# Kernel tuning notes

Measured on AMD Instinct MI355X. Metric: run time of the kernel, lower is better.

The kernel has to match this reference:

```python
import jax, jax.numpy as jnp
import numpy as np

N_NODES = 50000
N_EDGES = 800000
IN_CH = 128
OUT_CH = 64
HEADS = 2
NEG_SLOPE = 0.2


def _gat_conv(x, src, dst, W, a_src, a_dst, b, n):
    """PyG-style GATConv (eval mode: no dropout), self-loops already appended.
    x: [n, F_in]; W: [F_in, H*C]; a_src/a_dst: [H, C]; b: [H*C]."""
    H, C = a_src.shape
    h = (x @ W).reshape(n, H, C)                       # [n, H, C]
    alpha_src = jnp.sum(h * a_src, axis=-1)            # [n, H]
    alpha_dst = jnp.sum(h * a_dst, axis=-1)            # [n, H]
    e = alpha_src[src] + alpha_dst[dst]                # [E, H]
    e = jnp.where(e > 0, e, NEG_SLOPE * e)             # LeakyReLU(0.2)
    # neighbor-wise (destination-grouped) softmax, numerically stable
    m = jax.ops.segment_max(e, dst, num_segments=n)
    e = jnp.exp(e - m[dst])
    denom = jax.ops.segment_sum(e, dst, num_segments=n)
    alpha = e / (denom[dst] + 1e-16)                   # [E, H]
    out = jax.ops.segment_sum(alpha[:, :, None] * h[src], dst, num_segments=n)
    return out.reshape(n, H * C) + b


def setup_inputs() -> dict:
    key = jax.random.key(0)
    ks = jax.random.split(key, 12)
    s = 0.08  # glorot-ish scale
    x = jax.random.normal(ks[0], (N_NODES, IN_CH), dtype=jnp.float32)
    edge_index = jax.random.randint(ks[1], (2, N_EDGES), 0, N_NODES, dtype=jnp.int64)
    H, O = HEADS, OUT_CH
    return {
        "x": x,
        "edge_index": edge_index,
        "W1": jax.random.normal(ks[2], (IN_CH, H * 2 * O), dtype=jnp.float32) * s,
        "a_src1": jax.random.normal(ks[3], (H, 2 * O), dtype=jnp.float32) * s,
        "a_dst1": jax.random.normal(ks[4], (H, 2 * O), dtype=jnp.float32) * s,
        "b1": jnp.zeros((H * 2 * O,), dtype=jnp.float32),
        "W_mu": jax.random.normal(ks[5], (2 * O * H, H * O), dtype=jnp.float32) * s,
        "a_src_mu": jax.random.normal(ks[6], (H, O), dtype=jnp.float32) * s,
        "a_dst_mu": jax.random.normal(ks[7], (H, O), dtype=jnp.float32) * s,
        "b_mu": jnp.zeros((H * O,), dtype=jnp.float32),
        "W_ls": jax.random.normal(ks[8], (2 * O * H, H * O), dtype=jnp.float32) * s,
        "a_src_ls": jax.random.normal(ks[9], (H, O), dtype=jnp.float32) * s,
        "a_dst_ls": jax.random.normal(ks[10], (H, O), dtype=jnp.float32) * s,
        "b_ls": jnp.zeros((H * O,), dtype=jnp.float32),
    }


def reference(x, edge_index, W1, a_src1, a_dst1, b1,
              W_mu, a_src_mu, a_dst_mu, b_mu,
              W_ls, a_src_ls, a_dst_ls, b_ls):
    n = x.shape[0]
    loop = jnp.arange(n, dtype=edge_index.dtype)
    src = jnp.concatenate([edge_index[0], loop])  # PyG add_self_loops=True
    dst = jnp.concatenate([edge_index[1], loop])
    x1 = jax.nn.elu(_gat_conv(x, src, dst, W1, a_src1, a_dst1, b1, n))
    mu = _gat_conv(x1, src, dst, W_mu, a_src_mu, a_dst_mu, b_mu, n)
    logstd = _gat_conv(x1, src, dst, W_ls, a_src_ls, a_dst_ls, b_ls, n)
    return (mu, logstd)
```

## Files before the change

### kernel.cpp

```cpp
#include <hip/hip_runtime.h>


typedef unsigned short u16;
typedef unsigned int u32;
typedef _Float16 f16;
typedef f16 f16x8 __attribute__((ext_vector_type(8)));
typedef float f32x4v __attribute__((ext_vector_type(4)));

__device__ __forceinline__ u16 f2h(float f) {
    union { f16 h; u16 u; } t;
    t.h = (f16)f;
    return t.u;
}
__device__ __forceinline__ float4 loadh4(const u16* __restrict__ p, size_t i) {
    union { uint2 u; f16 h[4]; } t;
    t.u = *(const uint2*)(p + i);
    return make_float4((float)t.h[0], (float)t.h[1], (float)t.h[2], (float)t.h[3]);
}
__device__ __forceinline__ void store4(float* __restrict__ p, size_t i, float4 v) {
    *(float4*)(p + i) = v;
}
__device__ __forceinline__ void store4(u16* __restrict__ p, size_t i, float4 v) {
    union { uint2 u; f16 h[4]; } t;
    t.h[0] = (f16)v.x; t.h[1] = (f16)v.y; t.h[2] = (f16)v.z; t.h[3] = (f16)v.w;
    *(uint2*)(p + i) = t.u;
}

__global__ __launch_bounds__(256) void k_detect(const u32* __restrict__ ebuf,
                                                int* __restrict__ flag) {
    __shared__ int nz;
    if (threadIdx.x == 0) nz = 0;
    __syncthreads();
    if (ebuf[2 * threadIdx.x + 1] != 0u) atomicAdd(&nz, 1);
    __syncthreads();
    if (threadIdx.x == 0) *flag = (nz == 0) ? 1 : 0;
}

__global__ __launch_bounds__(256) void k_extract(const u32* __restrict__ ebuf, int E,
                                                 const int* __restrict__ flag,
                                                 int* __restrict__ se,
                                                 int* __restrict__ de,
                                                 int* __restrict__ deg) {
    int e = blockIdx.x * 256 + threadIdx.x;
    if (e >= E) return;
    int s, d;
    if (*flag) {
        s = (int)ebuf[2 * (size_t)e];
        d = (int)ebuf[2 * ((size_t)E + (size_t)e)];
    } else {
        s = (int)ebuf[e];
        d = (int)ebuf[(size_t)E + (size_t)e];
    }
    se[e] = s;
    de[e] = d;
    atomicAdd(&deg[d], 1);
}

__global__ __launch_bounds__(256) void k_scan_a(const int* __restrict__ deg, int n,
                                                int* __restrict__ bsum) {
    __shared__ int s[256];
    int i = blockIdx.x * 256 + threadIdx.x;
    s[threadIdx.x] = (i < n) ? deg[i] : 0;
    __syncthreads();
    for (int st = 128; st > 0; st >>= 1) {
        if (threadIdx.x < st) s[threadIdx.x] += s[threadIdx.x + st];
        __syncthreads();
    }
    if (threadIdx.x == 0) bsum[blockIdx.x] = s[0];
}

__global__ __launch_bounds__(256) void k_scan_b(int* __restrict__ bsum, int nb) {
    __shared__ int s[256];
    int t = threadIdx.x;
    int v = (t < nb) ? bsum[t] : 0;
    s[t] = v;
    __syncthreads();
    for (int off = 1; off < 256; off <<= 1) {
        int add = (t >= off) ? s[t - off] : 0;
        __syncthreads();
        s[t] += add;
        __syncthreads();
    }
    if (t < nb) bsum[t] = s[t] - v;
}

__global__ __launch_bounds__(256) void k_scan_c(const int* __restrict__ deg, int n,
                                                const int* __restrict__ bsum,
                                                int* __restrict__ rowptr,
                                                int* __restrict__ cursor, int E) {
    __shared__ int s[256];
    int t = threadIdx.x;
    int i = blockIdx.x * 256 + t;
    int v = (i < n) ? deg[i] : 0;
    s[t] = v;
    __syncthreads();
    for (int off = 1; off < 256; off <<= 1) {
        int add = (t >= off) ? s[t - off] : 0;
        __syncthreads();
        s[t] += add;
        __syncthreads();
    }
    if (i < n) {
        int ex = bsum[blockIdx.x] + s[t] - v;
        rowptr[i] = ex;
        cursor[i] = ex;
    }
    if (i == 0) rowptr[n] = E;
}

__global__ __launch_bounds__(256) void k_fill(const int* __restrict__ src,
                                              const int* __restrict__ dst, int E,
                                              int* __restrict__ cursor,
                                              int* __restrict__ csr_src,
                                              int* __restrict__ csr_dst) {
    int e = blockIdx.x * 256 + threadIdx.x;
    if (e < E) {
        int d = dst[e];
        int slot = atomicAdd(&cursor[d], 1);
        csr_src[slot] = src[e];
        csr_dst[slot] = d;
    }
}

__global__ __launch_bounds__(256) void k_cvt(const float* __restrict__ in,
                                             u16* __restrict__ out, int nElem) {
    int i = (blockIdx.x * 256 + threadIdx.x) * 4;
    if (i >= nElem) return;
    float4 v = *(const float4*)(in + i);
    store4(out, i, v);
}

__global__ __launch_bounds__(256) void k_tw(const float* __restrict__ Wl,
                                            const float* __restrict__ Wr, int split,
                                            int K, u16* __restrict__ Wt) {
    int idx = blockIdx.x * 256 + threadIdx.x;
    if (idx >= 256 * K) return;
    int c = idx / K, k = idx - c * K;
    float v;
    if (split == 256)
        v = Wl[(size_t)k * 256 + c];
    else
        v = (c < 128) ? Wl[(size_t)k * 128 + c] : Wr[(size_t)k * 128 + (c - 128)];
    Wt[idx] = f2h(v);
}

template <int NS>
__global__ __launch_bounds__(256) void k_w(const int* __restrict__ csr_src,
                                           const int* __restrict__ csr_dst,
                                           const float* __restrict__ as,
                                           const float* __restrict__ ad,
                                           float* __restrict__ wp, int E) {
    int i = blockIdx.x * 256 + threadIdx.x;
    if (i >= E) return;
    int s = csr_src[i], d = csr_dst[i];
    if (NS == 2) {
        float2 a = *(const float2*)(as + (size_t)s * 2);
        float2 b = *(const float2*)(ad + (size_t)d * 2);
        float e0 = a.x + b.x, e1 = a.y + b.y;
        e0 = fmaxf(e0, 0.2f * e0);
        e1 = fmaxf(e1, 0.2f * e1);
        wp[i] = __expf(e0);
        wp[(size_t)E + i] = __expf(e1);
    } else {
        float4 a = *(const float4*)(as + (size_t)s * 4);
        float4 b = *(const float4*)(ad + (size_t)d * 4);
        float e0 = a.x + b.x, e1 = a.y + b.y, e2 = a.z + b.z, e3 = a.w + b.w;
        e0 = fmaxf(e0, 0.2f * e0);
        e1 = fmaxf(e1, 0.2f * e1);
        e2 = fmaxf(e2, 0.2f * e2);
        e3 = fmaxf(e3, 0.2f * e3);
        wp[i] = __expf(e0);
        wp[(size_t)E + i] = __expf(e1);
        wp[2 * (size_t)E + i] = __expf(e2);
        wp[3 * (size_t)E + i] = __expf(e3);
    }
}

template <int K, int ALOGW>
__global__ __launch_bounds__(256) void k_gemm_mfma(
    const u16* __restrict__ Ah, const u16* __restrict__ Wt, u16* __restrict__ out,
    float* __restrict__ as_out, float* __restrict__ ad_out,
    const float* __restrict__ alo, const float* __restrict__ ahi,
    const float* __restrict__ dlo, const float* __restrict__ dhi, int M) {
    __shared__ u16 Bs[256 * 40];
    const int tid = threadIdx.x;
    const int wave = tid >> 6;
    const int lane = tid & 63;
    const int li = lane & 15;
    const int quad = lane >> 4;
    const int r0 = blockIdx.x * 64 + wave * 16;
    int arowi = r0 + li;
    if (arowi >= M) arowi = M - 1;
    const u16* arow = Ah + (size_t)arowi * K + quad * 8;

    f32x4v acc[16];
#pragma unroll
    for (int ct = 0; ct < 16; ct++) acc[ct] = (f32x4v)(0.f);

    for (int t = 0; t < K; t += 32) {
        __syncthreads();
        {
            const u16* src = Wt + (size_t)tid * K + t;
            u16* dst = Bs + tid * 40;
            uint4 v0 = ((const uint4*)src)[0];
            uint4 v1 = ((const uint4*)src)[1];
            uint4 v2 = ((const uint4*)src)[2];
            uint4 v3 = ((const uint4*)src)[3];
            ((uint4*)dst)[0] = v0;
            ((uint4*)(dst + 8))[0] = v1;
            ((uint4*)(dst + 16))[0] = v2;
            ((uint4*)(dst + 24))[0] = v3;
        }
        __syncthreads();
        f16x8 a = *(const f16x8*)(arow + t);
#pragma unroll
        for (int ct = 0; ct < 16; ct++) {
            f16x8 b = *(const f16x8*)(Bs + (ct * 16 + li) * 40 + quad * 8);
            acc[ct] = __builtin_amdgcn_mfma_f32_16x16x32_f16(a, b, acc[ct], 0, 0, 0);
        }
    }

#pragma unroll
    for (int reg = 0; reg < 4; reg++) {
        int grow = r0 + quad * 4 + reg;
        if (grow < M) {
            u16* orow = out + (size_t)grow * 256 + li;
#pragma unroll
            for (int ct = 0; ct < 16; ct++) orow[ct * 16] = f2h(acc[ct][reg]);
        }
    }

    const int NS = 64 >> ALOGW;
    const int SH = ALOGW - 2;
    float aw[16], dw[16];
#pragma unroll
    for (int ct = 0; ct < 16; ct++) {
        int col = ct * 16 + li;
        aw[ct] = (col < 128) ? alo[col] : ahi[col - 128];
        dw[ct] = (col < 128) ? dlo[col] : dhi[col - 128];
    }
#pragma unroll
    for (int reg = 0; reg < 4; reg++) {
        float s[4] = {0.f, 0.f, 0.f, 0.f};
        float d[4] = {0.f, 0.f, 0.f, 0.f};
#pragma unroll
        for (int ct = 0; ct < 16; ct++) {
            int sl = ct >> SH;
            s[sl] += acc[ct][reg] * aw[ct];
            d[sl] += acc[ct][reg] * dw[ct];
        }
#pragma unroll
        for (int sl = 0; sl < NS; sl++) {
#pragma unroll
            for (int m = 1; m <= 8; m <<= 1) {
                s[sl] += __shfl_xor(s[sl], m, 64);
                d[sl] += __shfl_xor(d[sl], m, 64);
            }
        }
        int grow = r0 + quad * 4 + reg;
        if (li == 0 && grow < M) {
#pragma unroll
            for (int sl = 0; sl < NS; sl++) {
                as_out[(size_t)grow * NS + sl] = s[sl];
                ad_out[(size_t)grow * NS + sl] = d[sl];
            }
        }
    }
}

template <int LOGW, int MODE, typename OT>
__global__ __launch_bounds__(256) void k_agg4(
    const u16* __restrict__ h, const int* __restrict__ rowptr,
    const int* __restrict__ csr_src, const float* __restrict__ wp,
    const float* __restrict__ as, const float* __restrict__ ad,
    const float* __restrict__ b_lo, const float* __restrict__ b_hi,
    OT* __restrict__ outp, int n, int nGrp, int E) {
    const int NS = 64 >> LOGW;
    const int bid = blockIdx.x;
    const int xcd = bid & 7;
    const int half = xcd >> 2;
    const int grp = (bid >> 3) * 4 + (xcd & 3);
    if (grp >= nGrp) return;
    const int lane = threadIdx.x & 63;
    const int sub = lane >> 5;
    const int sl = lane & 31;
    const int wid0 = grp * 8 + (threadIdx.x >> 6) * 2 + sub;
    const bool ok = wid0 < n;
    const int wid = ok ? wid0 : (n - 1);
    const int col = half * 128 + sl * 4;
    const int slot = col >> (LOGW + 2);
    const float* __restrict__ wpl = wp + (size_t)slot * E;

    float e = as[(size_t)wid * NS + slot] + ad[(size_t)wid * NS + slot];
    e = fmaxf(e, 0.2f * e);
    float w = __expf(e);
    float denom = w;
    float4 hv = loadh4(h, (size_t)wid * 256 + col);
    float acc0 = w * hv.x, acc1 = w * hv.y, acc2 = w * hv.z, acc3 = w * hv.w;

    int rb = 0, re = 0;
    if (ok) { rb = rowptr[wid0]; re = rowptr[wid0 + 1]; }
    int p = rb;
    for (; p + 8 <= re; p += 8) {
        int4 sA = *(const int4*)(csr_src + p);
        int4 sB = *(const int4*)(csr_src + p + 4);
        float4 wA = *(const float4*)(wpl + p);
        float4 wB = *(const float4*)(wpl + p + 4);
        float4 h0 = loadh4(h, (size_t)sA.x * 256 + col);
        float4 h1 = loadh4(h, (size_t)sA.y * 256 + col);
        float4 h2 = loadh4(h, (size_t)sA.z * 256 + col);
        float4 h3 = loadh4(h, (size_t)sA.w * 256 + col);
        float4 h4 = loadh4(h, (size_t)sB.x * 256 + col);
        float4 h5 = loadh4(h, (size_t)sB.y * 256 + col);
        float4 h6 = loadh4(h, (size_t)sB.z * 256 + col);
        float4 h7 = loadh4(h, (size_t)sB.w * 256 + col);
        denom += (wA.x + wA.y + wA.z + wA.w) + (wB.x + wB.y + wB.z + wB.w);
        acc0 += wA.x * h0.x + wA.y * h1.x + wA.z * h2.x + wA.w * h3.x +
                wB.x * h4.x + wB.y * h5.x + wB.z * h6.x + wB.w * h7.x;
        acc1 += wA.x * h0.y + wA.y * h1.y + wA.z * h2.y + wA.w * h3.y +
                wB.x * h4.y + wB.y * h5.y + wB.z * h6.y + wB.w * h7.y;
        acc2 += wA.x * h0.z + wA.y * h1.z + wA.z * h2.z + wA.w * h3.z +
                wB.x * h4.z + wB.y * h5.z + wB.z * h6.z + wB.w * h7.z;
        acc3 += wA.x * h0.w + wA.y * h1.w + wA.z * h2.w + wA.w * h3.w +
                wB.x * h4.w + wB.y * h5.w + wB.z * h6.w + wB.w * h7.w;
    }
    for (; p + 4 <= re; p += 4) {
        int4 sA = *(const int4*)(csr_src + p);
        float4 wA = *(const float4*)(wpl + p);
        float4 h0 = loadh4(h, (size_t)sA.x * 256 + col);
        float4 h1 = loadh4(h, (size_t)sA.y * 256 + col);
        float4 h2 = loadh4(h, (size_t)sA.z * 256 + col);
        float4 h3 = loadh4(h, (size_t)sA.w * 256 + col);
        denom += (wA.x + wA.y) + (wA.z + wA.w);
        acc0 += wA.x * h0.x + wA.y * h1.x + wA.z * h2.x + wA.w * h3.x;
        acc1 += wA.x * h0.y + wA.y * h1.y + wA.z * h2.y + wA.w * h3.y;
        acc2 += wA.x * h0.z + wA.y * h1.z + wA.z * h2.z + wA.w * h3.z;
        acc3 += wA.x * h0.w + wA.y * h1.w + wA.z * h2.w + wA.w * h3.w;
    }
    for (; p < re; ++p) {
        int s = csr_src[p];
        float ww = wpl[p];
        float4 hh = loadh4(h, (size_t)s * 256 + col);
        denom += ww;
        acc0 += ww * hh.x;
        acc1 += ww * hh.y;
        acc2 += ww * hh.z;
        acc3 += ww * hh.w;
    }
    float inv = 1.0f / (denom + 1e-16f);

    const float* bp = half ? b_hi : b_lo;
    const int ci = sl * 4;
    float4 bv = *(const float4*)(bp + ci);
    float v0 = acc0 * inv + bv.x;
    float v1 = acc1 * inv + bv.y;
    float v2 = acc2 * inv + bv.z;
    float v3 = acc3 * inv + bv.w;

    if (!ok) return;
    if (MODE == 0) {
        v0 = v0 > 0.f ? v0 : expm1f(v0);
        v1 = v1 > 0.f ? v1 : expm1f(v1);
        v2 = v2 > 0.f ? v2 : expm1f(v2);
        v3 = v3 > 0.f ? v3 : expm1f(v3);
        store4((u16*)outp, (size_t)wid0 * 256 + col, make_float4(v0, v1, v2, v3));
    } else {
        size_t base = half ? ((size_t)n * 128 + (size_t)wid0 * 128 + ci)
                           : ((size_t)wid0 * 128 + ci);
        store4((float*)outp, base, make_float4(v0, v1, v2, v3));
    }
}

extern "C" void kernel_launch(void* const* d_in, const int* in_sizes, int n_in,
                              void* d_out, int out_size, void* d_ws, size_t ws_size,
                              hipStream_t stream) {
    const float* x = (const float*)d_in[0];
    const u32* ebuf = (const u32*)d_in[1];
    const float* W1 = (const float*)d_in[2];
    const float* a_src1 = (const float*)d_in[3];
    const float* a_dst1 = (const float*)d_in[4];
    const float* b1 = (const float*)d_in[5];
    const float* W_mu = (const float*)d_in[6];
    const float* a_src_mu = (const float*)d_in[7];
    const float* a_dst_mu = (const float*)d_in[8];
    const float* b_mu = (const float*)d_in[9];
    const float* W_ls = (const float*)d_in[10];
    const float* a_src_ls = (const float*)d_in[11];
    const float* a_dst_ls = (const float*)d_in[12];
    const float* b_ls = (const float*)d_in[13];

    const int n = in_sizes[0] / 128;
    const int E = in_sizes[1] / 2;

    char* base = (char*)d_ws;
    size_t off = 0;
    auto alloc = [&](size_t b) -> char* {
        char* p = base + off;
        off = (off + b + 255) & ~(size_t)255;
        return p;
    };
    int* rowptr = (int*)alloc((size_t)(n + 1) * 4);
    int* cursor = (int*)alloc((size_t)n * 4);
    int* csr = (int*)alloc((size_t)E * 4);
    int* csrd = (int*)alloc((size_t)E * 4);
    int* bsum = (int*)alloc(256 * 4);
    int* eflag = (int*)alloc(256);
    int* se = (int*)alloc((size_t)E * 4);
    int* de = (int*)alloc((size_t)E * 4);
    float* as = (float*)alloc((size_t)n * 4 * 4);
    float* ad = (float*)alloc((size_t)n * 4 * 4);
    float* wp = (float*)alloc((size_t)E * 4 * 4);
    u16* W1t = (u16*)alloc(256 * 128 * 2);
    u16* Wt2 = (u16*)alloc(256 * 256 * 2);
    u16* x1h = (u16*)alloc((size_t)n * 256 * 2);
    u16* xh = x1h;
    u16* h = (u16*)alloc((size_t)n * 256 * 2);

    const int nb = (n + 255) / 256;
    const int eg = (E + 255) / 256;
    const int gg = (n + 63) / 64;
    const int nGrp = (n + 7) / 8;
    const int aggGrid = 8 * ((nGrp + 3) / 4);

    hipMemsetAsync(cursor, 0, (size_t)n * 4, stream);
    k_detect<<<1, 256, 0, stream>>>(ebuf, eflag);
    k_extract<<<eg, 256, 0, stream>>>(ebuf, E, eflag, se, de, cursor);
    k_scan_a<<<nb, 256, 0, stream>>>(cursor, n, bsum);
    k_scan_b<<<1, 256, 0, stream>>>(bsum, nb);
    k_scan_c<<<nb, 256, 0, stream>>>(cursor, n, bsum, rowptr, cursor, E);
    k_fill<<<eg, 256, 0, stream>>>(se, de, E, cursor, csr, csrd);

    k_cvt<<<(n * 128 / 4 + 255) / 256, 256, 0, stream>>>(x, xh, n * 128);
    k_tw<<<(256 * 128 + 255) / 256, 256, 0, stream>>>(W1, W1, 256, 128, W1t);
    k_tw<<<(256 * 256 + 255) / 256, 256, 0, stream>>>(W_mu, W_ls, 128, 256, Wt2);

    k_gemm_mfma<128, 5><<<gg, 256, 0, stream>>>(xh, W1t, h, as, ad, a_src1,
                                                a_src1 + 128, a_dst1, a_dst1 + 128,
                                                n);
    k_w<2><<<eg, 256, 0, stream>>>(csr, csrd, as, ad, wp, E);
    k_agg4<5, 0, u16><<<aggGrid, 256, 0, stream>>>(h, rowptr, csr, wp, as, ad, b1,
                                                   b1 + 128, x1h, n, nGrp, E);

    k_gemm_mfma<256, 4><<<gg, 256, 0, stream>>>(x1h, Wt2, h, as, ad, a_src_mu,
                                                a_src_ls, a_dst_mu, a_dst_ls, n);
    k_w<4><<<eg, 256, 0, stream>>>(csr, csrd, as, ad, wp, E);
    k_agg4<4, 1, float><<<aggGrid, 256, 0, stream>>>(h, rowptr, csr, wp, as, ad,
                                                     b_mu, b_ls, (float*)d_out, n,
                                                     nGrp, E);
}
```

Baseline: 391.8 us.

## Degree-sort aggregation rows, fuse fp32 input conversion into GEMM, prefetch tiles

Three changes at once. A degree histogram and counting sort build a permutation so each aggregation wave processes nodes of similar degree, aimed at reducing loop-count divergence between the two half-waves. The separate fp32-to-fp16 conversion kernel for x is removed, and the first GEMM loads fp32 rows directly and converts them in registers. The GEMM K-loop now register-prefetches the next W and A tiles before the compute barrier, to overlap global loads with MFMA work. In exchange there are three extra small kernels, and writes scattered by the permutation lose locality.

```diff
diff --git a/kernel.cpp b/kernel.cpp
--- a/kernel.cpp
+++ b/kernel.cpp
@@ -56,6 +56,38 @@
     atomicAdd(&deg[d], 1);
 }
 
+__global__ __launch_bounds__(256) void k_hist(const int* __restrict__ deg, int n,
+                                              int* __restrict__ hist) {
+    __shared__ int hs[64];
+    if (threadIdx.x < 64) hs[threadIdx.x] = 0;
+    __syncthreads();
+    int i = blockIdx.x * 256 + threadIdx.x;
+    if (i < n) atomicAdd(&hs[min(deg[i], 63)], 1);
+    __syncthreads();
+    if (threadIdx.x < 64 && hs[threadIdx.x]) atomicAdd(&hist[threadIdx.x], hs[threadIdx.x]);
+}
+
+__global__ void k_hscan(const int* __restrict__ hist, int* __restrict__ hcur) {
+    int t = threadIdx.x;
+    int h0 = hist[t];
+    int v = h0;
+    for (int off = 1; off < 64; off <<= 1) {
+        int u = __shfl_up(v, off, 64);
+        if (t >= off) v += u;
+    }
+    hcur[t] = v - h0;
+}
+
+__global__ __launch_bounds__(256) void k_perm(const int* __restrict__ deg, int n,
+                                              int* __restrict__ hcur,
+                                              int* __restrict__ perm) {
+    int i = blockIdx.x * 256 + threadIdx.x;
+    if (i < n) {
+        int pos = atomicAdd(&hcur[min(deg[i], 63)], 1);
+        perm[pos] = i;
+    }
+}
+
 __global__ __launch_bounds__(256) void k_scan_a(const int* __restrict__ deg, int n,
                                                 int* __restrict__ bsum) {
     __shared__ int s[256];
@@ -120,14 +152,6 @@
         csr_src[slot] = src[e];
         csr_dst[slot] = d;
     }
-}
-
-__global__ __launch_bounds__(256) void k_cvt(const float* __restrict__ in,
-                                             u16* __restrict__ out, int nElem) {
-    int i = (blockIdx.x * 256 + threadIdx.x) * 4;
-    if (i >= nElem) return;
-    float4 v = *(const float4*)(in + i);
-    store4(out, i, v);
 }
 
 __global__ __launch_bounds__(256) void k_tw(const float* __restrict__ Wl,
@@ -176,9 +200,9 @@
     }
 }
 
-template <int K, int ALOGW>
+template <int K, int ALOGW, bool AF32>
 __global__ __launch_bounds__(256) void k_gemm_mfma(
-    const u16* __restrict__ Ah, const u16* __restrict__ Wt, u16* __restrict__ out,
+    const void* __restrict__ Av, const u16* __restrict__ Wt, u16* __restrict__ out,
     float* __restrict__ as_out, float* __restrict__ ad_out,
     const float* __restrict__ alo, const float* __restrict__ ahi,
     const float* __restrict__ dlo, const float* __restrict__ dhi, int M) {
@@ -191,28 +215,64 @@
     const int r0 = blockIdx.x * 64 + wave * 16;
     int arowi = r0 + li;
     if (arowi >= M) arowi = M - 1;
-    const u16* arow = Ah + (size_t)arowi * K + quad * 8;
+    const u16* arow16 = (const u16*)Av + (AF32 ? 0 : (size_t)arowi * K + quad * 8);
+    const float* arow32 = (const float*)Av + (AF32 ? (size_t)arowi * K + quad * 8 : 0);
 
     f32x4v acc[16];
 #pragma unroll
     for (int ct = 0; ct < 16; ct++) acc[ct] = (f32x4v)(0.f);
 
+    const u16* wrow = Wt + (size_t)tid * K;
+    u16* dstp = Bs + tid * 40;
+    uint4 sv0 = ((const uint4*)wrow)[0];
+    uint4 sv1 = ((const uint4*)(wrow + 8))[0];
+    uint4 sv2 = ((const uint4*)(wrow + 16))[0];
+    uint4 sv3 = ((const uint4*)(wrow + 24))[0];
+    uint4 apf0, apf1;
+    if (AF32) {
+        apf0 = *(const uint4*)(arow32);
+        apf1 = *(const uint4*)(arow32 + 4);
+    } else {
+        apf0 = *(const uint4*)(arow16);
+        apf1 = apf0;
+    }
+
     for (int t = 0; t < K; t += 32) {
-        __syncthreads();
-        {
-            const u16* src = Wt + (size_t)tid * K + t;
-            u16* dst = Bs + tid * 40;
-            uint4 v0 = ((const uint4*)src)[0];
-            uint4 v1 = ((const uint4*)src)[1];
-            uint4 v2 = ((const uint4*)src)[2];
-            uint4 v3 = ((const uint4*)src)[3];
-            ((uint4*)dst)[0] = v0;
-            ((uint4*)(dst + 8))[0] = v1;
-            ((uint4*)(dst + 16))[0] = v2;
-            ((uint4*)(dst + 24))[0] = v3;
-        }
-        __syncthreads();
-        f16x8 a = *(const f16x8*)(arow + t);
+        asm volatile("s_waitcnt lgkmcnt(0)" ::: "memory");
+        __builtin_amdgcn_s_barrier();
+        ((uint4*)dstp)[0] = sv0;
+        ((uint4*)(dstp + 8))[0] = sv1;
+        ((uint4*)(dstp + 16))[0] = sv2;
+        ((uint4*)(dstp + 24))[0] = sv3;
+        f16x8 a;
+        if (AF32) {
+            union { uint4 u; float f[4]; } ua, ub;
+            ua.u = apf0;
+            ub.u = apf1;
+            a[0] = (f16)ua.f[0]; a[1] = (f16)ua.f[1];
+            a[2] = (f16)ua.f[2]; a[3] = (f16)ua.f[3];
+            a[4] = (f16)ub.f[0]; a[5] = (f16)ub.f[1];
+            a[6] = (f16)ub.f[2]; a[7] = (f16)ub.f[3];
+        } else {
+            union { uint4 u; f16x8 h; } uh;
+            uh.u = apf0;
+            a = uh.h;
+        }
+        if (t + 32 < K) {
+            const u16* s2 = wrow + t + 32;
+            sv0 = ((const uint4*)s2)[0];
+            sv1 = ((const uint4*)(s2 + 8))[0];
+            sv2 = ((const uint4*)(s2 + 16))[0];
+            sv3 = ((const uint4*)(s2 + 24))[0];
+            if (AF32) {
+                apf0 = *(const uint4*)(arow32 + t + 32);
+                apf1 = *(const uint4*)(arow32 + t + 36);
+            } else {
+                apf0 = *(const uint4*)(arow16 + t + 32);
+            }
+        }
+        asm volatile("s_waitcnt lgkmcnt(0)" ::: "memory");
+        __builtin_amdgcn_s_barrier();
 #pragma unroll
         for (int ct = 0; ct < 16; ct++) {
             f16x8 b = *(const f16x8*)(Bs + (ct * 16 + li) * 40 + quad * 8);
@@ -274,7 +334,7 @@
     const int* __restrict__ csr_src, const float* __restrict__ wp,
     const float* __restrict__ as, const float* __restrict__ ad,
     const float* __restrict__ b_lo, const float* __restrict__ b_hi,
-    OT* __restrict__ outp, int n, int nGrp, int E) {
+    const int* __restrict__ perm, OT* __restrict__ outp, int n, int nGrp, int E) {
     const int NS = 64 >> LOGW;
     const int bid = blockIdx.x;
     const int xcd = bid & 7;
@@ -284,9 +344,9 @@
     const int lane = threadIdx.x & 63;
     const int sub = lane >> 5;
     const int sl = lane & 31;
-    const int wid0 = grp * 8 + (threadIdx.x >> 6) * 2 + sub;
-    const bool ok = wid0 < n;
-    const int wid = ok ? wid0 : (n - 1);
+    const int idx = grp * 8 + (threadIdx.x >> 6) * 2 + sub;
+    const bool ok = idx < n;
+    const int wid = perm[ok ? idx : 0];
     const int col = half * 128 + sl * 4;
     const int slot = col >> (LOGW + 2);
     const float* __restrict__ wpl = wp + (size_t)slot * E;
@@ -299,7 +359,7 @@
     float acc0 = w * hv.x, acc1 = w * hv.y, acc2 = w * hv.z, acc3 = w * hv.w;
 
     int rb = 0, re = 0;
-    if (ok) { rb = rowptr[wid0]; re = rowptr[wid0 + 1]; }
+    if (ok) { rb = rowptr[wid]; re = rowptr[wid + 1]; }
     int p = rb;
     for (; p + 8 <= re; p += 8) {
         int4 sA = *(const int4*)(csr_src + p);
@@ -363,10 +423,10 @@
         v1 = v1 > 0.f ? v1 : expm1f(v1);
         v2 = v2 > 0.f ? v2 : expm1f(v2);
         v3 = v3 > 0.f ? v3 : expm1f(v3);
-        store4((u16*)outp, (size_t)wid0 * 256 + col, make_float4(v0, v1, v2, v3));
+        store4((u16*)outp, (size_t)wid * 256 + col, make_float4(v0, v1, v2, v3));
     } else {
-        size_t base = half ? ((size_t)n * 128 + (size_t)wid0 * 128 + ci)
-                           : ((size_t)wid0 * 128 + ci);
+        size_t base = half ? ((size_t)n * 128 + (size_t)wid * 128 + ci)
+                           : ((size_t)wid * 128 + ci);
         store4((float*)outp, base, make_float4(v0, v1, v2, v3));
     }
 }
@@ -407,13 +467,15 @@
     int* eflag = (int*)alloc(256);
     int* se = (int*)alloc((size_t)E * 4);
     int* de = (int*)alloc((size_t)E * 4);
+    int* perm = (int*)alloc((size_t)n * 4);
+    int* hist = (int*)alloc(64 * 4);
+    int* hcur = (int*)alloc(64 * 4);
     float* as = (float*)alloc((size_t)n * 4 * 4);
     float* ad = (float*)alloc((size_t)n * 4 * 4);
     float* wp = (float*)alloc((size_t)E * 4 * 4);
     u16* W1t = (u16*)alloc(256 * 128 * 2);
     u16* Wt2 = (u16*)alloc(256 * 256 * 2);
     u16* x1h = (u16*)alloc((size_t)n * 256 * 2);
-    u16* xh = x1h;
     u16* h = (u16*)alloc((size_t)n * 256 * 2);
 
     const int nb = (n + 255) / 256;
@@ -423,28 +485,32 @@
     const int aggGrid = 8 * ((nGrp + 3) / 4);
 
     hipMemsetAsync(cursor, 0, (size_t)n * 4, stream);
+    hipMemsetAsync(hist, 0, 64 * 4, stream);
     k_detect<<<1, 256, 0, stream>>>(ebuf, eflag);
     k_extract<<<eg, 256, 0, stream>>>(ebuf, E, eflag, se, de, cursor);
+    k_hist<<<nb, 256, 0, stream>>>(cursor, n, hist);
+    k_hscan<<<1, 64, 0, stream>>>(hist, hcur);
+    k_perm<<<nb, 256, 0, stream>>>(cursor, n, hcur, perm);
     k_scan_a<<<nb, 256, 0, stream>>>(cursor, n, bsum);
     k_scan_b<<<1, 256, 0, stream>>>(bsum, nb);
     k_scan_c<<<nb, 256, 0, stream>>>(cursor, n, bsum, rowptr, cursor, E);
     k_fill<<<eg, 256, 0, stream>>>(se, de, E, cursor, csr, csrd);
 
-    k_cvt<<<(n * 128 / 4 + 255) / 256, 256, 0, stream>>>(x, xh, n * 128);
     k_tw<<<(256 * 128 + 255) / 256, 256, 0, stream>>>(W1, W1, 256, 128, W1t);
     k_tw<<<(256 * 256 + 255) / 256, 256, 0, stream>>>(W_mu, W_ls, 128, 256, Wt2);
 
-    k_gemm_mfma<128, 5><<<gg, 256, 0, stream>>>(xh, W1t, h, as, ad, a_src1,
-                                                a_src1 + 128, a_dst1, a_dst1 + 128,
-                                                n);
+    k_gemm_mfma<128, 5, true><<<gg, 256, 0, stream>>>(x, W1t, h, as, ad, a_src1,
+                                                      a_src1 + 128, a_dst1,
+                                                      a_dst1 + 128, n);
     k_w<2><<<eg, 256, 0, stream>>>(csr, csrd, as, ad, wp, E);
     k_agg4<5, 0, u16><<<aggGrid, 256, 0, stream>>>(h, rowptr, csr, wp, as, ad, b1,
-                                                   b1 + 128, x1h, n, nGrp, E);
-
-    k_gemm_mfma<256, 4><<<gg, 256, 0, stream>>>(x1h, Wt2, h, as, ad, a_src_mu,
-                                                a_src_ls, a_dst_mu, a_dst_ls, n);
+                                                   b1 + 128, perm, x1h, n, nGrp, E);
+
+    k_gemm_mfma<256, 4, false><<<gg, 256, 0, stream>>>(x1h, Wt2, h, as, ad,
+                                                       a_src_mu, a_src_ls,
+                                                       a_dst_mu, a_dst_ls, n);
     k_w<4><<<eg, 256, 0, stream>>>(csr, csrd, as, ad, wp, E);
     k_agg4<4, 1, float><<<aggGrid, 256, 0, stream>>>(h, rowptr, csr, wp, as, ad,
-                                                     b_mu, b_ls, (float*)d_out, n,
-                                                     nGrp, E);
-}
+                                                     b_mu, b_ls, perm,
+                                                     (float*)d_out, n, nGrp, E);
+}
```

New measurement: 538.5 us. +37.4%, slower.
